# Kernel tuning notes

Hardware: AMD Instinct MI355X
Metric: run time of the kernel (lower is better)

The kernel has to match this reference:

```python
import jax, jax.numpy as jnp
import numpy as np

NHEAD = 8
ATTN_EPS = 1e-6
LN_EPS = 1e-5


def _layernorm(y, g, b):
    mu = jnp.mean(y, axis=-1, keepdims=True)
    var = jnp.var(y, axis=-1, keepdims=True)
    return (y - mu) * jax.lax.rsqrt(var + LN_EPS) * g + b


def setup_inputs() -> dict:
    key = jax.random.key(0)
    ks = jax.random.split(key, 6)
    B, L, D = 2, 8192, 1024
    s = 1.0 / np.sqrt(D)
    return {
        "x": jax.random.normal(ks[0], (B, L, D), jnp.float32),
        "Wq": jax.random.normal(ks[1], (D, D), jnp.float32) * s,
        "Wm": jax.random.normal(ks[2], (D, D), jnp.float32) * s,
        "W1": jax.random.normal(ks[3], (D, 2 * D), jnp.float32) * s,
        "W2": jax.random.normal(ks[4], (2 * D, D), jnp.float32) * (1.0 / np.sqrt(2 * D)),
        "g1": jnp.ones((D,), jnp.float32),
        "b1": jnp.zeros((D,), jnp.float32),
        "g2": jnp.ones((D,), jnp.float32),
        "b2": jnp.zeros((D,), jnp.float32),
    }


def reference(x, Wq, Wm, W1, W2, g1, b1, g2, b2):
    B, L, D = x.shape
    H = NHEAD
    d = D // H
    # NOTE: original forward uses q_proj for query, key AND value (faithful).
    q = (x @ Wq).reshape(B, L, H, d)  # [B,L,H,d]
    feat = jax.nn.elu(q) + 1.0        # elu feature map, shared by Q and K
    Q = feat
    K = feat
    V = q / L                          # value = value / v_length
    # KV outer-product sum over sequence: [B,H,d,d]
    KV = jnp.einsum('nshd,nshv->nhdv', K, V)
    # normalizer Z: [B,L,H]
    Ksum = K.sum(axis=1)               # [B,H,d]
    Z = 1.0 / (jnp.einsum('nlhd,nhd->nlh', Q, Ksum) + ATTN_EPS)
    msg = jnp.einsum('nlhd,nhdv,nlh->nlhv', Q, KV, Z) * L  # [B,L,H,d]
    msg = msg.reshape(B, L, D) @ Wm    # merge heads
    x = x + _layernorm(msg, g1, b1)
    # NOTE: MLP is applied to `message`, not the updated x (faithful to source).
    mlp = jax.nn.relu(msg @ W1) @ W2
    x = x + _layernorm(mlp, g2, b2)
    return x
```

## Files before the change

kernel.cpp:

```cpp
#include <hip/hip_runtime.h>
#include <hip/hip_bf16.h>
#include <stdint.h>

#define AS1 __attribute__((address_space(1)))
#define AS3 __attribute__((address_space(3)))

typedef __bf16 bf16x8 __attribute__((ext_vector_type(8)));
typedef __bf16 bf16x2 __attribute__((ext_vector_type(2)));
typedef float  f32x4  __attribute__((ext_vector_type(4)));

static constexpr int kL   = 8192;
static constexpr int kD   = 1024;
static constexpr int kM   = 2 * kL;
static constexpr int kNCH = 16;
static constexpr int kSCH = kL / kNCH;

__device__ __forceinline__ void async_cp16(__bf16* lds, const __bf16* g) {
    __builtin_amdgcn_global_load_lds((AS1 uint32_t*)g, (AS3 uint32_t*)lds, 16, 0, 0);
}

__device__ __forceinline__ float elu1f(float x) {
    return x > 0.0f ? x + 1.0f : __expf(x);
}

template <int M0>
__device__ __forceinline__ void mfma16(f32x4 (&acc)[8][4], const bf16x8 (&af)[4],
                                       const bf16x8 (&bq)[4]) {
#pragma unroll
    for (int i = 0; i < 4; ++i)
#pragma unroll
        for (int n = 0; n < 4; ++n)
            acc[M0 + i][n] = __builtin_amdgcn_mfma_f32_16x16x32_bf16(af[i], bq[n], acc[M0 + i][n], 0, 0, 0);
}

template <int EPI>
__global__ __launch_bounds__(512, 2) void gemm256(const __bf16* __restrict__ A,
                                                  const __bf16* __restrict__ Bt,
                                                  __bf16* __restrict__ C,
                                                  int M, int N, int K) {
    __shared__ __bf16 As[32768];
    __shared__ __bf16 Bs[32768];
    const int tid  = threadIdx.x;
    const int w    = tid >> 6;
    const int l    = tid & 63;
    const int quad = l >> 4;
    const int l16  = l & 15;
    const int wm   = w >> 2;
    const int wn   = w & 3;
    const int row0 = blockIdx.x * 256;
    const int col0 = blockIdx.y * 256;

    const int srow = l >> 2;
    const int sc   = ((l & 3) - (srow >> 1)) & 3;
    const __bf16* Ag0 = A  + (size_t)(row0 + w * 32 + srow) * K + sc * 8;
    const __bf16* Bg0 = Bt + (size_t)(col0 + w * 32 + srow) * K + sc * 8;
    const size_t r16K = (size_t)16 * K;
    const int NT = K >> 6;

    const int fpos = ((quad + (l16 >> 1)) & 3) * 8;
    const int arow = wm * 4096 + l16 * 32 + fpos;
    const int brow = wn * 2048 + l16 * 32 + fpos;

    f32x4 acc[8][4] = {};

    auto stage_h = [&](int ts, int hh) {
        if (ts >= NT) return;
        const int off = (ts & 1) * 16384 + (hh >> 1) * 8192 + w * 1024;
        const int ko  = ts * 64 + (hh >> 1) * 32;
        if ((hh & 1) == 0) {
            async_cp16(&As[off], Ag0 + ko);
            async_cp16(&As[off + 512], Ag0 + ko + r16K);
        } else {
            async_cp16(&Bs[off], Bg0 + ko);
            async_cp16(&Bs[off + 512], Bg0 + ko + r16K);
        }
    };

    stage_h(0, 0); stage_h(0, 1); stage_h(0, 2); stage_h(0, 3);
    asm volatile("s_waitcnt vmcnt(4)" ::: "memory");
    stage_h(1, 0); stage_h(1, 1); stage_h(1, 2);
    asm volatile("s_waitcnt vmcnt(6)" ::: "memory");
    __builtin_amdgcn_s_barrier();

    for (int t = 0; t < NT; ++t) {
        const int bo = (t & 1) * 16384;
        bf16x8 af[4], bq[4];

#pragma unroll
        for (int i = 0; i < 4; ++i) af[i] = *(const bf16x8*)&As[bo + arow + i * 512];
#pragma unroll
        for (int n = 0; n < 4; ++n) bq[n] = *(const bf16x8*)&Bs[bo + brow + n * 512];
        stage_h(t + 1, 3);
        __builtin_amdgcn_s_barrier();
        asm volatile("s_waitcnt lgkmcnt(0)" ::: "memory");
        __builtin_amdgcn_sched_barrier(0);
        __builtin_amdgcn_s_setprio(1);
        mfma16<0>(acc, af, bq);
        __builtin_amdgcn_s_setprio(0);
        __builtin_amdgcn_s_barrier();

#pragma unroll
        for (int i = 0; i < 4; ++i) af[i] = *(const bf16x8*)&As[bo + arow + 2048 + i * 512];
        stage_h(t + 2, 0);
        __builtin_amdgcn_s_barrier();
        asm volatile("s_waitcnt lgkmcnt(0)" ::: "memory");
        __builtin_amdgcn_sched_barrier(0);
        __builtin_amdgcn_s_setprio(1);
        mfma16<4>(acc, af, bq);
        __builtin_amdgcn_s_setprio(0);
        __builtin_amdgcn_s_barrier();

#pragma unroll
        for (int i = 0; i < 4; ++i) af[i] = *(const bf16x8*)&As[bo + 8192 + arow + i * 512];
#pragma unroll
        for (int n = 0; n < 4; ++n) bq[n] = *(const bf16x8*)&Bs[bo + 8192 + brow + n * 512];
        stage_h(t + 2, 1);
        __builtin_amdgcn_s_barrier();
        asm volatile("s_waitcnt lgkmcnt(0)" ::: "memory");
        __builtin_amdgcn_sched_barrier(0);
        __builtin_amdgcn_s_setprio(1);
        mfma16<0>(acc, af, bq);
        __builtin_amdgcn_s_setprio(0);
        __builtin_amdgcn_s_barrier();

#pragma unroll
        for (int i = 0; i < 4; ++i) af[i] = *(const bf16x8*)&As[bo + 8192 + arow + 2048 + i * 512];
        stage_h(t + 2, 2);
        __builtin_amdgcn_s_barrier();
        asm volatile("s_waitcnt lgkmcnt(0)" ::: "memory");
        __builtin_amdgcn_sched_barrier(0);
        __builtin_amdgcn_s_setprio(1);
        mfma16<4>(acc, af, bq);
        __builtin_amdgcn_s_setprio(0);
        if (t + 2 < NT)       { asm volatile("s_waitcnt vmcnt(6)" ::: "memory"); }
        else if (t + 2 == NT) { asm volatile("s_waitcnt vmcnt(0)" ::: "memory"); }
        __builtin_amdgcn_s_barrier();
    }

#pragma unroll
    for (int m = 0; m < 8; ++m) {
        const int rowb = row0 + wm * 128 + m * 16 + quad * 4;
#pragma unroll
        for (int n = 0; n < 4; ++n) {
            const int col = col0 + wn * 64 + n * 16 + l16;
#pragma unroll
            for (int r = 0; r < 4; ++r) {
                float v = acc[m][n][r];
                if (EPI == 1) v = v > 0.0f ? v : 0.0f;
                C[(size_t)(rowb + r) * N + col] = (__bf16)v;
            }
        }
    }
    (void)M;
}

__global__ __launch_bounds__(256) void cvt_f2b(const float* __restrict__ in,
                                               __bf16* __restrict__ out) {
    const size_t i = ((size_t)blockIdx.x * 256 + threadIdx.x) * 8;
    f32x4 a = *(const f32x4*)(in + i);
    f32x4 b = *(const f32x4*)(in + i + 4);
    bf16x8 o;
#pragma unroll
    for (int j = 0; j < 4; ++j) { o[j] = (__bf16)a[j]; o[4 + j] = (__bf16)b[j]; }
    *(bf16x8*)(out + i) = o;
}

__global__ __launch_bounds__(256) void transpose_f2b(const float* __restrict__ in,
                                                     __bf16* __restrict__ out,
                                                     int R, int Ccols) {
    __shared__ __bf16 tile[32][33];
    const int bc = blockIdx.x * 32;
    const int br = blockIdx.y * 32;
    const int tx = threadIdx.x & 31;
    const int ty = threadIdx.x >> 5;
#pragma unroll
    for (int i = ty; i < 32; i += 8)
        tile[i][tx] = (__bf16)in[(size_t)(br + i) * Ccols + bc + tx];
    __syncthreads();
#pragma unroll
    for (int i = ty; i < 32; i += 8)
        out[(size_t)(bc + i) * R + br + tx] = tile[tx][i];
}

__global__ __launch_bounds__(256) void transpose_q(__bf16* __restrict__ q_io,
                                                   __bf16* __restrict__ qT,
                                                   __bf16* __restrict__ fT) {
    __shared__ __bf16 qs[64 * 130];
    __shared__ __bf16 fs[64 * 130];
    const int bh = blockIdx.x, b = bh >> 3, h = bh & 7;
    const int s0 = blockIdx.y * 64;
    const int t = threadIdx.x;
    const size_t rowbase = (size_t)b * 8388608 + (size_t)h * 128;

#pragma unroll
    for (int c = 0; c < 4; ++c) {
        const int id = c * 256 + t;
        const int r = id >> 4, col = (id & 15) * 8;
        __bf16* gp = q_io + rowbase + (size_t)(s0 + r) * 1024 + col;
        bf16x8 qv = *(const bf16x8*)gp;
        bf16x8 fv;
#pragma unroll
        for (int j = 0; j < 8; ++j) fv[j] = (__bf16)elu1f((float)qv[j]);
        *(bf16x8*)gp = fv;
        const int lb = r * 130 + col;
#pragma unroll
        for (int p = 0; p < 4; ++p) {
            bf16x2 qp = { qv[2 * p], qv[2 * p + 1] };
            bf16x2 fp_ = { fv[2 * p], fv[2 * p + 1] };
            *(bf16x2*)&qs[lb + 2 * p] = qp;
            *(bf16x2*)&fs[lb + 2 * p] = fp_;
        }
    }
    __syncthreads();

    const size_t ob = (size_t)bh * (128 * 8192) + s0;
#pragma unroll
    for (int c = 0; c < 4; ++c) {
        const int id = c * 256 + t;
        const int dk = id >> 3, sch = id & 7;
        bf16x8 ov, fo;
#pragma unroll
        for (int j = 0; j < 8; ++j) {
            ov[j] = qs[(sch * 8 + j) * 130 + dk];
            fo[j] = fs[(sch * 8 + j) * 130 + dk];
        }
        *(bf16x8*)(qT + ob + (size_t)dk * 8192 + sch * 8) = ov;
        *(bf16x8*)(fT + ob + (size_t)dk * 8192 + sch * 8) = fo;
    }
}

__global__ __launch_bounds__(256) void kv_gemm(const __bf16* __restrict__ fT,
                                               const __bf16* __restrict__ qT,
                                               float* __restrict__ KVpart,
                                               float* __restrict__ Kspart) {
    __shared__ __bf16 As[2][128 * 32];
    __shared__ __bf16 Bs[2][128 * 32];
    const int tid  = threadIdx.x;
    const int wave = tid >> 6, lane = tid & 63;
    const int quad = lane >> 4, l16 = lane & 15;
    const int wm = wave & 1, wn = wave >> 1;
    const int bh = blockIdx.x, ch = blockIdx.y;

    f32x4 acc[4][4] = {};
    float ksacc[4] = {};

    const int srow = lane >> 2;
    const int sk8  = ((lane & 3) - (srow >> 1)) & 3;
    const size_t base = (size_t)bh * (128 * 8192) + ch * kSCH + sk8 * 8;
    const __bf16* Ag0 = fT + base + (size_t)(wave * 32 + srow) * 8192;
    const __bf16* Bg0 = qT + base + (size_t)(wave * 32 + srow) * 8192;
    const size_t r16 = (size_t)16 * 8192;
    const int ldsw = wave * 1024;
    const int fp = ((quad + (l16 >> 1)) & 3) * 8;
    const int frow = l16 * 32 + fp;
    const int nk = kSCH / 32;
    {
        async_cp16(&As[0][ldsw], Ag0);
        async_cp16(&As[0][ldsw + 512], Ag0 + r16);
        async_cp16(&Bs[0][ldsw], Bg0);
        async_cp16(&Bs[0][ldsw + 512], Bg0 + r16);
    }
    for (int k = 0; k < nk; ++k) {
        __syncthreads();
        if (k + 1 < nk) {
            const int nb = (k + 1) & 1;
            const int ko = (k + 1) << 5;
            async_cp16(&As[nb][ldsw], Ag0 + ko);
            async_cp16(&As[nb][ldsw + 512], Ag0 + r16 + ko);
            async_cp16(&Bs[nb][ldsw], Bg0 + ko);
            async_cp16(&Bs[nb][ldsw + 512], Bg0 + r16 + ko);
        }
        const __bf16* Asb = As[k & 1];
        const __bf16* Bsb = Bs[k & 1];
        bf16x8 af[4], bfr[4];
#pragma unroll
        for (int i = 0; i < 4; ++i)
            af[i] = *(const bf16x8*)&Asb[(wm * 4 + i) * 512 + frow];
#pragma unroll
        for (int j = 0; j < 4; ++j)
            bfr[j] = *(const bf16x8*)&Bsb[(wn * 4 + j) * 512 + frow];
        if (wn == 0) {
#pragma unroll
            for (int i = 0; i < 4; ++i)
#pragma unroll
                for (int j = 0; j < 8; ++j) ksacc[i] += (float)af[i][j];
        }
#pragma unroll
        for (int i = 0; i < 4; ++i)
#pragma unroll
            for (int j = 0; j < 4; ++j)
                acc[i][j] = __builtin_amdgcn_mfma_f32_16x16x32_bf16(af[i], bfr[j], acc[i][j], 0, 0, 0);
    }

    float* outp = KVpart + (((size_t)bh * kNCH + ch) << 14);
#pragma unroll
    for (int i = 0; i < 4; ++i) {
        const int rowb = wm * 64 + i * 16 + quad * 4;
#pragma unroll
        for (int j = 0; j < 4; ++j) {
            const int col = wn * 64 + j * 16 + l16;
#pragma unroll
            for (int r = 0; r < 4; ++r)
                outp[(rowb + r) * 128 + col] = acc[i][j][r];
        }
    }
    if (wn == 0) {
#pragma unroll
        for (int i = 0; i < 4; ++i) {
            float v = ksacc[i];
            v += __shfl_xor(v, 16);
            v += __shfl_xor(v, 32);
            if (quad == 0)
                Kspart[((size_t)bh * kNCH + ch) * 128 + wm * 64 + i * 16 + l16] = v;
        }
    }
}

__global__ __launch_bounds__(256) void reduce_kv(const float* __restrict__ KVpart,
                                                 const float* __restrict__ Kspart,
                                                 __bf16* __restrict__ KVbT,
                                                 float* __restrict__ Ksum) {
    const int t = threadIdx.x;
    if (blockIdx.x < 1024) {
        const size_t o = (size_t)blockIdx.x * 256 + t;
        const size_t bh = o >> 14;
        const size_t rem = o & 16383;
        float s = 0.f;
#pragma unroll 4
        for (int ch = 0; ch < kNCH; ++ch)
            s += KVpart[((bh * kNCH + ch) << 14) + rem];
        const int dk = (int)(rem >> 7), dv = (int)(rem & 127);
        KVbT[(bh << 14) + dv * 128 + dk] = (__bf16)s;
    } else {
        const int o = (blockIdx.x - 1024) * 256 + t;
        const int bh = o >> 7;
        const int dk = o & 127;
        float s = 0.f;
#pragma unroll 4
        for (int ch = 0; ch < kNCH; ++ch)
            s += Kspart[(bh * kNCH + ch) * 128 + dk];
        Ksum[o] = s;
    }
}

__global__ __launch_bounds__(256) void msg_gemm(const __bf16* __restrict__ featG,
                                                const __bf16* __restrict__ KVbT,
                                                const float* __restrict__ Ks,
                                                __bf16* __restrict__ msg) {
    __shared__ __bf16 As[2][128 * 32];
    __shared__ __bf16 Bs[2][128 * 32];
    __shared__ float KsS[128];
    __shared__ float Zsh[128];
    const int tid  = threadIdx.x;
    const int wave = tid >> 6, lane = tid & 63;
    const int quad = lane >> 4, l16 = lane & 15;
    const int wm = wave & 1, wn = wave >> 1;
    const int bh = blockIdx.x, b = bh >> 3, h = bh & 7;
    const int row0 = blockIdx.y * 128;

    if (tid < 32)
        *(f32x4*)&KsS[tid * 4] = *(const f32x4*)(Ks + bh * 128 + tid * 4);

    f32x4 acc[4][4] = {};
    float zacc[4] = {};
    const int srow = lane >> 2;
    const int sk8  = ((lane & 3) - (srow >> 1)) & 3;
    const __bf16* Ag0 = featG + (size_t)b * 8388608 + (size_t)(row0 + wave * 32 + srow) * 1024 + h * 128 + sk8 * 8;
    const __bf16* Bg0 = KVbT + ((size_t)bh << 14) + (wave * 32 + srow) * 128 + sk8 * 8;
    const size_t rA16 = (size_t)16 * 1024;
    const size_t rB16 = (size_t)16 * 128;
    const int ldsw = wave * 1024;
    const int fp = ((quad + (l16 >> 1)) & 3) * 8;
    const int frow = l16 * 32 + fp;
    const int nk = 4;
    {
        async_cp16(&As[0][ldsw], Ag0);
        async_cp16(&As[0][ldsw + 512], Ag0 + rA16);
        async_cp16(&Bs[0][ldsw], Bg0);
        async_cp16(&Bs[0][ldsw + 512], Bg0 + rB16);
    }
    for (int k = 0; k < nk; ++k) {
        __syncthreads();
        if (k + 1 < nk) {
            const int nb = (k + 1) & 1;
            const int ko = (k + 1) << 5;
            async_cp16(&As[nb][ldsw], Ag0 + ko);
            async_cp16(&As[nb][ldsw + 512], Ag0 + rA16 + ko);
            async_cp16(&Bs[nb][ldsw], Bg0 + ko);
            async_cp16(&Bs[nb][ldsw + 512], Bg0 + rB16 + ko);
        }
        const __bf16* Asb = As[k & 1];
        const __bf16* Bsb = Bs[k & 1];
        bf16x8 af[4], bfr[4];
#pragma unroll
        for (int i = 0; i < 4; ++i)
            af[i] = *(const bf16x8*)&Asb[(wm * 4 + i) * 512 + frow];
#pragma unroll
        for (int j = 0; j < 4; ++j)
            bfr[j] = *(const bf16x8*)&Bsb[(wn * 4 + j) * 512 + frow];
        {
            f32x4 k0 = *(const f32x4*)&KsS[k * 32 + quad * 8];
            f32x4 k1 = *(const f32x4*)&KsS[k * 32 + quad * 8 + 4];
#pragma unroll
            for (int i = 0; i < 4; ++i) {
#pragma unroll
                for (int j = 0; j < 4; ++j) {
                    zacc[i] += (float)af[i][j] * k0[j];
                    zacc[i] += (float)af[i][4 + j] * k1[j];
                }
            }
        }
#pragma unroll
        for (int i = 0; i < 4; ++i)
#pragma unroll
            for (int j = 0; j < 4; ++j)
                acc[i][j] = __builtin_amdgcn_mfma_f32_16x16x32_bf16(af[i], bfr[j], acc[i][j], 0, 0, 0);
    }

#pragma unroll
    for (int i = 0; i < 4; ++i) {
        float v = zacc[i];
        v += __shfl_xor(v, 16);
        v += __shfl_xor(v, 32);
        if (wn == 0 && quad == 0)
            Zsh[wm * 64 + i * 16 + l16] = 1.0f / (v + 1e-6f);
    }
    __syncthreads();

    const size_t obase = (size_t)b * 8388608 + (size_t)h * 128;
#pragma unroll
    for (int i = 0; i < 4; ++i) {
        const int lr0 = wm * 64 + i * 16 + quad * 4;
#pragma unroll
        for (int j = 0; j < 4; ++j) {
            const int col = wn * 64 + j * 16 + l16;
#pragma unroll
            for (int r = 0; r < 4; ++r) {
                const float v = acc[i][j][r] * Zsh[lr0 + r];
                msg[obase + (size_t)(row0 + lr0 + r) * 1024 + col] = (__bf16)v;
            }
        }
    }
}

template <int BF16BASE>
__global__ __launch_bounds__(256) void ln_res(const void* __restrict__ basep,
                                              const __bf16* __restrict__ y,
                                              const float* __restrict__ g,
                                              const float* __restrict__ bvec,
                                              float* __restrict__ out) {
    const int wave = threadIdx.x >> 6, lane = threadIdx.x & 63;
    const int row = blockIdx.x * 4 + wave;
    const size_t ro = (size_t)row * kD + lane * 16;
    bf16x8 y0 = *(const bf16x8*)(y + ro);
    bf16x8 y1 = *(const bf16x8*)(y + ro + 8);
    float v[16];
    float s = 0.f, sq = 0.f;
#pragma unroll
    for (int j = 0; j < 8; ++j) { v[j] = (float)y0[j]; v[8 + j] = (float)y1[j]; }
#pragma unroll
    for (int j = 0; j < 16; ++j) { s += v[j]; sq += v[j] * v[j]; }
#pragma unroll
    for (int m = 1; m < 64; m <<= 1) { s += __shfl_xor(s, m); sq += __shfl_xor(sq, m); }
    const float mu = s * (1.0f / 1024.0f);
    float var = sq * (1.0f / 1024.0f) - mu * mu;
    if (var < 0.f) var = 0.f;
    const float rstd = rsqrtf(var + 1e-5f);
    const int go = lane * 16;
    float bs[16];
    if (BF16BASE) {
        bf16x8 b0 = *(const bf16x8*)((const __bf16*)basep + ro);
        bf16x8 b1 = *(const bf16x8*)((const __bf16*)basep + ro + 8);
#pragma unroll
        for (int j = 0; j < 8; ++j) { bs[j] = (float)b0[j]; bs[8 + j] = (float)b1[j]; }
    } else {
#pragma unroll
        for (int j = 0; j < 4; ++j) {
            f32x4 bb = *(const f32x4*)((const float*)basep + ro + j * 4);
#pragma unroll
            for (int r = 0; r < 4; ++r) bs[j * 4 + r] = bb[r];
        }
    }
#pragma unroll
    for (int j = 0; j < 4; ++j) {
        f32x4 gg = *(const f32x4*)(g + go + j * 4);
        f32x4 be = *(const f32x4*)(bvec + go + j * 4);
        f32x4 o;
#pragma unroll
        for (int r = 0; r < 4; ++r)
            o[r] = bs[j * 4 + r] + (v[j * 4 + r] - mu) * rstd * gg[r] + be[r];
        *(f32x4*)(out + ro + j * 4) = o;
    }
}

extern "C" void kernel_launch(void* const* d_in, const int* in_sizes, int n_in,
                              void* d_out, int out_size, void* d_ws, size_t ws_size,
                              hipStream_t stream) {
    const float* x  = (const float*)d_in[0];
    const float* Wq = (const float*)d_in[1];
    const float* Wm = (const float*)d_in[2];
    const float* W1 = (const float*)d_in[3];
    const float* W2 = (const float*)d_in[4];
    const float* g1 = (const float*)d_in[5];
    const float* b1 = (const float*)d_in[6];
    const float* g2 = (const float*)d_in[7];
    const float* b2 = (const float*)d_in[8];
    float* out = (float*)d_out;

    const size_t BLD = (size_t)kM * kD;
    __bf16* q    = (__bf16*)d_ws;
    __bf16* msg  = q + BLD;
    __bf16* hbuf = msg + BLD;
    __bf16* WqT  = hbuf + 2 * BLD;
    __bf16* WmT  = WqT + 1048576;
    __bf16* W1T  = WmT + 1048576;
    __bf16* W2T  = W1T + 2097152;
    __bf16* KVb  = W2T + 2097152;
    float* KVpart = (float*)(KVb + 262144);
    float* Kspart = KVpart + (size_t)kNCH * 16 * 16384;
    float* Ksum   = Kspart + (size_t)16 * kNCH * 128;
    const size_t need = ((char*)(Ksum + 2048)) - (char*)d_ws;
    if (ws_size < need) return;

    __bf16* xb   = hbuf;
    __bf16* qT   = hbuf + BLD;
    __bf16* fT   = msg;
    __bf16* featG = q;
    __bf16* msg2 = q;
    __bf16* mlp  = msg;

    const dim3 blk(256);
    const dim3 blk5(512);

    cvt_f2b<<<dim3((unsigned)(BLD / 2048)), blk, 0, stream>>>(x, xb);
    transpose_f2b<<<dim3(32, 32), blk, 0, stream>>>(Wq, WqT, kD, kD);
    transpose_f2b<<<dim3(32, 32), blk, 0, stream>>>(Wm, WmT, kD, kD);
    transpose_f2b<<<dim3(64, 32), blk, 0, stream>>>(W1, W1T, kD, 2048);
    transpose_f2b<<<dim3(32, 64), blk, 0, stream>>>(W2, W2T, 2048, kD);

    gemm256<0><<<dim3(kM / 256, kD / 256), blk5, 0, stream>>>(xb, WqT, q, kM, kD, kD);
    transpose_q<<<dim3(16, 128), blk, 0, stream>>>(q, qT, fT);
    kv_gemm<<<dim3(16, kNCH), blk, 0, stream>>>(fT, qT, KVpart, Kspart);
    reduce_kv<<<dim3(1032), blk, 0, stream>>>(KVpart, Kspart, KVb, Ksum);
    msg_gemm<<<dim3(16, kL / 128), blk, 0, stream>>>(featG, KVb, Ksum, msg);
    gemm256<0><<<dim3(kM / 256, kD / 256), blk5, 0, stream>>>(msg, WmT, msg2, kM, kD, kD);
    ln_res<1><<<dim3(kM / 4), blk, 0, stream>>>(xb, msg2, g1, b1, out);
    gemm256<1><<<dim3(kM / 256, 2048 / 256), blk5, 0, stream>>>(msg2, W1T, hbuf, kM, 2048, kD);
    gemm256<0><<<dim3(kM / 256, kD / 256), blk5, 0, stream>>>(hbuf, W2T, mlp, kM, kD, 2048);
    ln_res<0><<<dim3(kM / 4), blk, 0, stream>>>(out, mlp, g2, b2, out);
    (void)in_sizes; (void)n_in; (void)out_size;
}
```

Measured before the change: 468.7 us.

## Compute ELU feature on the fly and merge prep kernels into one launch

Moves the ELU+1 feature map out of the transpose kernel, which no longer writes a transposed feature copy or overwrites q in place. kv_gemm now loads only qT into LDS and applies ELU to the A fragments in registers, and msg_gemm does the same on the raw q fragments. The conversion of x and the four weight transposes are also merged into a single prep launch. This cuts global memory traffic and launch overhead, at the cost of recomputing exp in the GEMM inner loops.

```diff
diff --git a/kernel.cpp b/kernel.cpp
--- a/kernel.cpp
+++ b/kernel.cpp
@@ -21,6 +21,13 @@
 
 __device__ __forceinline__ float elu1f(float x) {
     return x > 0.0f ? x + 1.0f : __expf(x);
+}
+
+__device__ __forceinline__ bf16x8 elu8(bf16x8 v) {
+    bf16x8 r;
+#pragma unroll
+    for (int j = 0; j < 8; ++j) r[j] = (__bf16)elu1f((float)v[j]);
+    return r;
 }
 
 template <int M0>
@@ -154,25 +161,12 @@
     (void)M;
 }
 
-__global__ __launch_bounds__(256) void cvt_f2b(const float* __restrict__ in,
-                                               __bf16* __restrict__ out) {
-    const size_t i = ((size_t)blockIdx.x * 256 + threadIdx.x) * 8;
-    f32x4 a = *(const f32x4*)(in + i);
-    f32x4 b = *(const f32x4*)(in + i + 4);
-    bf16x8 o;
-#pragma unroll
-    for (int j = 0; j < 4; ++j) { o[j] = (__bf16)a[j]; o[4 + j] = (__bf16)b[j]; }
-    *(bf16x8*)(out + i) = o;
-}
-
-__global__ __launch_bounds__(256) void transpose_f2b(const float* __restrict__ in,
-                                                     __bf16* __restrict__ out,
-                                                     int R, int Ccols) {
-    __shared__ __bf16 tile[32][33];
-    const int bc = blockIdx.x * 32;
-    const int br = blockIdx.y * 32;
-    const int tx = threadIdx.x & 31;
-    const int ty = threadIdx.x >> 5;
+__device__ __forceinline__ void transpose_body(const float* __restrict__ in,
+                                               __bf16* __restrict__ out,
+                                               int R, int Ccols, int bx, int by,
+                                               int t, __bf16 (*tile)[33]) {
+    const int bc = bx * 32, br = by * 32;
+    const int tx = t & 31, ty = t >> 5;
 #pragma unroll
     for (int i = ty; i < 32; i += 8)
         tile[i][tx] = (__bf16)in[(size_t)(br + i) * Ccols + bc + tx];
@@ -182,11 +176,47 @@
         out[(size_t)(bc + i) * R + br + tx] = tile[tx][i];
 }
 
-__global__ __launch_bounds__(256) void transpose_q(__bf16* __restrict__ q_io,
-                                                   __bf16* __restrict__ qT,
-                                                   __bf16* __restrict__ fT) {
+__global__ __launch_bounds__(256) void prep(const float* __restrict__ x,
+                                            __bf16* __restrict__ xb,
+                                            const float* __restrict__ Wq,
+                                            __bf16* __restrict__ WqT,
+                                            const float* __restrict__ Wm,
+                                            __bf16* __restrict__ WmT,
+                                            const float* __restrict__ W1,
+                                            __bf16* __restrict__ W1T,
+                                            const float* __restrict__ W2,
+                                            __bf16* __restrict__ W2T) {
+    __shared__ __bf16 tile[32][33];
+    const int t = threadIdx.x;
+    int id = blockIdx.x;
+    if (id < 8192) {
+        const size_t i = ((size_t)id * 256 + t) * 8;
+        f32x4 a = *(const f32x4*)(x + i);
+        f32x4 b = *(const f32x4*)(x + i + 4);
+        bf16x8 o;
+#pragma unroll
+        for (int j = 0; j < 4; ++j) { o[j] = (__bf16)a[j]; o[4 + j] = (__bf16)b[j]; }
+        *(bf16x8*)(xb + i) = o;
+        return;
+    }
+    id -= 8192;
+    if (id < 1024) {
+        transpose_body(Wq, WqT, 1024, 1024, id & 31, id >> 5, t, tile);
+    } else if (id < 2048) {
+        const int i2 = id - 1024;
+        transpose_body(Wm, WmT, 1024, 1024, i2 & 31, i2 >> 5, t, tile);
+    } else if (id < 4096) {
+        const int i2 = id - 2048;
+        transpose_body(W1, W1T, 1024, 2048, i2 & 63, i2 >> 6, t, tile);
+    } else {
+        const int i2 = id - 4096;
+        transpose_body(W2, W2T, 2048, 1024, i2 & 31, i2 >> 5, t, tile);
+    }
+}
+
+__global__ __launch_bounds__(256) void transpose_q(const __bf16* __restrict__ q,
+                                                   __bf16* __restrict__ qT) {
     __shared__ __bf16 qs[64 * 130];
-    __shared__ __bf16 fs[64 * 130];
     const int bh = blockIdx.x, b = bh >> 3, h = bh & 7;
     const int s0 = blockIdx.y * 64;
     const int t = threadIdx.x;
@@ -196,19 +226,12 @@
     for (int c = 0; c < 4; ++c) {
         const int id = c * 256 + t;
         const int r = id >> 4, col = (id & 15) * 8;
-        __bf16* gp = q_io + rowbase + (size_t)(s0 + r) * 1024 + col;
-        bf16x8 qv = *(const bf16x8*)gp;
-        bf16x8 fv;
-#pragma unroll
-        for (int j = 0; j < 8; ++j) fv[j] = (__bf16)elu1f((float)qv[j]);
-        *(bf16x8*)gp = fv;
+        bf16x8 qv = *(const bf16x8*)(q + rowbase + (size_t)(s0 + r) * 1024 + col);
         const int lb = r * 130 + col;
 #pragma unroll
         for (int p = 0; p < 4; ++p) {
             bf16x2 qp = { qv[2 * p], qv[2 * p + 1] };
-            bf16x2 fp_ = { fv[2 * p], fv[2 * p + 1] };
             *(bf16x2*)&qs[lb + 2 * p] = qp;
-            *(bf16x2*)&fs[lb + 2 * p] = fp_;
         }
     }
     __syncthreads();
@@ -218,23 +241,17 @@
     for (int c = 0; c < 4; ++c) {
         const int id = c * 256 + t;
         const int dk = id >> 3, sch = id & 7;
-        bf16x8 ov, fo;
-#pragma unroll
-        for (int j = 0; j < 8; ++j) {
-            ov[j] = qs[(sch * 8 + j) * 130 + dk];
-            fo[j] = fs[(sch * 8 + j) * 130 + dk];
-        }
+        bf16x8 ov;
+#pragma unroll
+        for (int j = 0; j < 8; ++j) ov[j] = qs[(sch * 8 + j) * 130 + dk];
         *(bf16x8*)(qT + ob + (size_t)dk * 8192 + sch * 8) = ov;
-        *(bf16x8*)(fT + ob + (size_t)dk * 8192 + sch * 8) = fo;
-    }
-}
-
-__global__ __launch_bounds__(256) void kv_gemm(const __bf16* __restrict__ fT,
-                                               const __bf16* __restrict__ qT,
+    }
+}
+
+__global__ __launch_bounds__(256) void kv_gemm(const __bf16* __restrict__ qT,
                                                float* __restrict__ KVpart,
                                                float* __restrict__ Kspart) {
-    __shared__ __bf16 As[2][128 * 32];
-    __shared__ __bf16 Bs[2][128 * 32];
+    __shared__ __bf16 Qs[2][128 * 32];
     const int tid  = threadIdx.x;
     const int wave = tid >> 6, lane = tid & 63;
     const int quad = lane >> 4, l16 = lane & 15;
@@ -247,38 +264,32 @@
     const int srow = lane >> 2;
     const int sk8  = ((lane & 3) - (srow >> 1)) & 3;
     const size_t base = (size_t)bh * (128 * 8192) + ch * kSCH + sk8 * 8;
-    const __bf16* Ag0 = fT + base + (size_t)(wave * 32 + srow) * 8192;
-    const __bf16* Bg0 = qT + base + (size_t)(wave * 32 + srow) * 8192;
+    const __bf16* Qg0 = qT + base + (size_t)(wave * 32 + srow) * 8192;
     const size_t r16 = (size_t)16 * 8192;
     const int ldsw = wave * 1024;
     const int fp = ((quad + (l16 >> 1)) & 3) * 8;
     const int frow = l16 * 32 + fp;
     const int nk = kSCH / 32;
     {
-        async_cp16(&As[0][ldsw], Ag0);
-        async_cp16(&As[0][ldsw + 512], Ag0 + r16);
-        async_cp16(&Bs[0][ldsw], Bg0);
-        async_cp16(&Bs[0][ldsw + 512], Bg0 + r16);
+        async_cp16(&Qs[0][ldsw], Qg0);
+        async_cp16(&Qs[0][ldsw + 512], Qg0 + r16);
     }
     for (int k = 0; k < nk; ++k) {
         __syncthreads();
         if (k + 1 < nk) {
             const int nb = (k + 1) & 1;
             const int ko = (k + 1) << 5;
-            async_cp16(&As[nb][ldsw], Ag0 + ko);
-            async_cp16(&As[nb][ldsw + 512], Ag0 + r16 + ko);
-            async_cp16(&Bs[nb][ldsw], Bg0 + ko);
-            async_cp16(&Bs[nb][ldsw + 512], Bg0 + r16 + ko);
-        }
-        const __bf16* Asb = As[k & 1];
-        const __bf16* Bsb = Bs[k & 1];
+            async_cp16(&Qs[nb][ldsw], Qg0 + ko);
+            async_cp16(&Qs[nb][ldsw + 512], Qg0 + r16 + ko);
+        }
+        const __bf16* Qsb = Qs[k & 1];
         bf16x8 af[4], bfr[4];
 #pragma unroll
         for (int i = 0; i < 4; ++i)
-            af[i] = *(const bf16x8*)&Asb[(wm * 4 + i) * 512 + frow];
+            af[i] = elu8(*(const bf16x8*)&Qsb[(wm * 4 + i) * 512 + frow]);
 #pragma unroll
         for (int j = 0; j < 4; ++j)
-            bfr[j] = *(const bf16x8*)&Bsb[(wn * 4 + j) * 512 + frow];
+            bfr[j] = *(const bf16x8*)&Qsb[(wn * 4 + j) * 512 + frow];
         if (wn == 0) {
 #pragma unroll
             for (int i = 0; i < 4; ++i)
@@ -343,7 +354,7 @@
     }
 }
 
-__global__ __launch_bounds__(256) void msg_gemm(const __bf16* __restrict__ featG,
+__global__ __launch_bounds__(256) void msg_gemm(const __bf16* __restrict__ q,
                                                 const __bf16* __restrict__ KVbT,
                                                 const float* __restrict__ Ks,
                                                 __bf16* __restrict__ msg) {
@@ -365,7 +376,7 @@
     float zacc[4] = {};
     const int srow = lane >> 2;
     const int sk8  = ((lane & 3) - (srow >> 1)) & 3;
-    const __bf16* Ag0 = featG + (size_t)b * 8388608 + (size_t)(row0 + wave * 32 + srow) * 1024 + h * 128 + sk8 * 8;
+    const __bf16* Ag0 = q + (size_t)b * 8388608 + (size_t)(row0 + wave * 32 + srow) * 1024 + h * 128 + sk8 * 8;
     const __bf16* Bg0 = KVbT + ((size_t)bh << 14) + (wave * 32 + srow) * 128 + sk8 * 8;
     const size_t rA16 = (size_t)16 * 1024;
     const size_t rB16 = (size_t)16 * 128;
@@ -394,7 +405,7 @@
         bf16x8 af[4], bfr[4];
 #pragma unroll
         for (int i = 0; i < 4; ++i)
-            af[i] = *(const bf16x8*)&Asb[(wm * 4 + i) * 512 + frow];
+            af[i] = elu8(*(const bf16x8*)&Asb[(wm * 4 + i) * 512 + frow]);
 #pragma unroll
         for (int j = 0; j < 4; ++j)
             bfr[j] = *(const bf16x8*)&Bsb[(wn * 4 + j) * 512 + frow];
@@ -524,25 +535,19 @@
 
     __bf16* xb   = hbuf;
     __bf16* qT   = hbuf + BLD;
-    __bf16* fT   = msg;
-    __bf16* featG = q;
     __bf16* msg2 = q;
     __bf16* mlp  = msg;
 
     const dim3 blk(256);
     const dim3 blk5(512);
 
-    cvt_f2b<<<dim3((unsigned)(BLD / 2048)), blk, 0, stream>>>(x, xb);
-    transpose_f2b<<<dim3(32, 32), blk, 0, stream>>>(Wq, WqT, kD, kD);
-    transpose_f2b<<<dim3(32, 32), blk, 0, stream>>>(Wm, WmT, kD, kD);
-    transpose_f2b<<<dim3(64, 32), blk, 0, stream>>>(W1, W1T, kD, 2048);
-    transpose_f2b<<<dim3(32, 64), blk, 0, stream>>>(W2, W2T, 2048, kD);
+    prep<<<dim3(14336), blk, 0, stream>>>(x, xb, Wq, WqT, Wm, WmT, W1, W1T, W2, W2T);
 
     gemm256<0><<<dim3(kM / 256, kD / 256), blk5, 0, stream>>>(xb, WqT, q, kM, kD, kD);
-    transpose_q<<<dim3(16, 128), blk, 0, stream>>>(q, qT, fT);
-    kv_gemm<<<dim3(16, kNCH), blk, 0, stream>>>(fT, qT, KVpart, Kspart);
+    transpose_q<<<dim3(16, 128), blk, 0, stream>>>(q, qT);
+    kv_gemm<<<dim3(16, kNCH), blk, 0, stream>>>(qT, KVpart, Kspart);
     reduce_kv<<<dim3(1032), blk, 0, stream>>>(KVpart, Kspart, KVb, Ksum);
-    msg_gemm<<<dim3(16, kL / 128), blk, 0, stream>>>(featG, KVb, Ksum, msg);
+    msg_gemm<<<dim3(16, kL / 128), blk, 0, stream>>>(q, KVb, Ksum, msg);
     gemm256<0><<<dim3(kM / 256, kD / 256), blk5, 0, stream>>>(msg, WmT, msg2, kM, kD, kD);
     ln_res<1><<<dim3(kM / 4), blk, 0, stream>>>(xb, msg2, g1, b1, out);
     gemm256<1><<<dim3(kM / 256, 2048 / 256), blk5, 0, stream>>>(msg2, W1T, hbuf, kM, 2048, kD);
```

Result: faster. 450.3 us, median of 3 (-3.9%).
